# Kernel optimization log

Hardware: AMD Instinct MI355X
Metric: run time of the kernel (lower is better)

Reference implementation:

```python
import jax, jax.numpy as jnp
import numpy as np

DIM = 2048
HID = 1024
E = 16
TOP_K = 2
S_SHARED = 2


def setup_inputs() -> dict:
    key = jax.random.key(0)
    ks = jax.random.split(key, 6)
    scale = 0.02
    x = jax.random.normal(ks[0], (2, 2048, DIM), dtype=jnp.float32)
    gate_w = jax.random.normal(ks[1], (DIM, E), dtype=jnp.float32) * scale
    shared_w1 = jax.random.normal(ks[2], (S_SHARED, DIM, HID), dtype=jnp.float32) * scale
    shared_w2 = jax.random.normal(ks[3], (S_SHARED, HID, DIM), dtype=jnp.float32) * scale
    w1 = jax.random.normal(ks[4], (E, DIM, HID), dtype=jnp.float32) * scale
    w2 = jax.random.normal(ks[5], (E, HID, DIM), dtype=jnp.float32) * scale
    return {"x": x, "gate_w": gate_w, "shared_w1": shared_w1,
            "shared_w2": shared_w2, "w1": w1, "w2": w2}


def reference(x, gate_w, shared_w1, shared_w2, w1, w2):
    orig_shape = x.shape
    xf = x.reshape(-1, orig_shape[-1])  # [T, D]

    # Shared experts: sum of SiLU MLPs
    hs = jax.nn.silu(jnp.einsum('td,sdh->sth', xf, shared_w1))
    shared_out = jnp.einsum('sth,shd->td', hs, shared_w2)

    # Gating
    probs = jax.nn.softmax(xf @ gate_w, axis=-1)              # [T, E]
    weights, indices = jax.lax.top_k(probs, TOP_K)            # [T, K]
    weights = weights / weights.sum(axis=-1, keepdims=True)
    aux_loss = (probs.mean(axis=0) ** 2).sum() * E

    # Combine weights per (token, expert): top_k indices are distinct
    combine = (jax.nn.one_hot(indices, E, dtype=xf.dtype) *
               weights[..., None]).sum(axis=1)                # [T, E]

    # Dense all-expert compute (reference form of gather-GEMM-scatter)
    h = jax.nn.silu(jnp.einsum('td,edh->eth', xf, w1))        # [E, T, H]
    y = jnp.einsum('eth,ehd->etd', h, w2)                     # [E, T, D]
    routed_out = jnp.einsum('te,etd->td', combine, y)         # [T, D]

    out = (shared_out + routed_out).reshape(orig_shape)
    return out, aux_loss
```

## Files before the change

### kernel.cpp

```cpp
#include <hip/hip_runtime.h>
#include <math.h>

typedef unsigned short u16;
typedef __bf16 bf16x8 __attribute__((ext_vector_type(8)));
typedef float f32x4 __attribute__((ext_vector_type(4)));

#define T_TOK 4096
#define DIMD 2048
#define HIDD 1024
#define NEXP 16
#define RMAX 10240
#define MAXBLK 96
#define BM 128
#define BN 128
#define BK 32

__device__ __forceinline__ u16 f2b(float f) {
  unsigned u = __builtin_bit_cast(unsigned, f);
  unsigned r = (u + 0x7FFFu + ((u >> 16) & 1u)) >> 16;
  return (u16)r;
}

__device__ __forceinline__ void gld16(const void* g, void* l) {
  __builtin_amdgcn_global_load_lds(
      (const __attribute__((address_space(1))) void*)g,
      (__attribute__((address_space(3))) void*)l, 16, 0, 0);
}


__global__ void k_init(int* perm, int* cnt, int* fill) {
  int i = blockIdx.x * blockDim.x + threadIdx.x;
  if (i < RMAX) perm[i] = -1;
  if (i < NEXP) { cnt[i] = 0; fill[i] = 0; }
}

__global__ void k_cvt(const float* __restrict__ x, u16* __restrict__ xb) {
  const int i = blockIdx.x * blockDim.x + threadIdx.x;
  const float4 v = ((const float4*)x)[i];
  union { u16 u[4]; unsigned long long q; } t;
  t.u[0] = f2b(v.x); t.u[1] = f2b(v.y); t.u[2] = f2b(v.z); t.u[3] = f2b(v.w);
  ((unsigned long long*)xb)[i] = t.q;
}

__global__ __launch_bounds__(256)
void k_tr(const float* __restrict__ W, u16* __restrict__ Wt,
          int K, int N, long estride, int ld_out) {
  __shared__ float t[64][65];
  const int e = blockIdx.z;
  const float* Win = W + (size_t)e * (size_t)K * (size_t)N;
  u16* Wo = Wt + (size_t)e * (size_t)estride;
  const int n0 = blockIdx.x * 64, k0 = blockIdx.y * 64;
  const int r = threadIdx.x >> 4;
  const int c = (threadIdx.x & 15) * 4;
#pragma unroll
  for (int p = 0; p < 4; ++p) {
    const int kk = p * 16 + r;
    const float4 v = *(const float4*)&Win[(size_t)(k0 + kk) * N + n0 + c];
    t[kk][c] = v.x; t[kk][c + 1] = v.y; t[kk][c + 2] = v.z; t[kk][c + 3] = v.w;
  }
  __syncthreads();
#pragma unroll
  for (int p = 0; p < 4; ++p) {
    const int nn = p * 16 + r;
    ushort4 o;
    o.x = f2b(t[c + 0][nn]); o.y = f2b(t[c + 1][nn]);
    o.z = f2b(t[c + 2][nn]); o.w = f2b(t[c + 3][nn]);
    *(ushort4*)&Wo[(size_t)(n0 + nn) * ld_out + k0 + c] = o;
  }
}

__global__ __launch_bounds__(256)
void k_gate(const float* __restrict__ x, const float* __restrict__ gw,
            int* __restrict__ top2i, float* __restrict__ top2w,
            int* __restrict__ cnt, float* __restrict__ partial) {
  const int e = threadIdx.x & 15;
  const int tt = threadIdx.x >> 4;
  const int t = blockIdx.x * 16 + tt;
  const float* xp = x + (size_t)t * DIMD;
  float acc = 0.f;
#pragma unroll 8
  for (int k = 0; k < DIMD; ++k) acc = fmaf(xp[k], gw[k * NEXP + e], acc);
  __shared__ float lg[16][17];
  __shared__ float pr[16][17];
  lg[tt][e] = acc;
  __syncthreads();
  if (e == 0) {
    float l[16];
    float mx = -1e30f;
    for (int j = 0; j < 16; ++j) { l[j] = lg[tt][j]; mx = fmaxf(mx, l[j]); }
    float s = 0.f;
    for (int j = 0; j < 16; ++j) { l[j] = expf(l[j] - mx); s += l[j]; }
    const float inv = 1.f / s;
    float p1 = -1.f, p2 = -1.f; int i1 = 0, i2 = 0;
    for (int j = 0; j < 16; ++j) {
      const float p = l[j] * inv;
      pr[tt][j] = p;
      if (p > p1) { p2 = p1; i2 = i1; p1 = p; i1 = j; }
      else if (p > p2) { p2 = p; i2 = j; }
    }
    const float wsum = p1 + p2;
    top2i[t * 2 + 0] = i1;
    top2i[t * 2 + 1] = i2;
    top2w[t * 2 + 0] = p1 / wsum;
    top2w[t * 2 + 1] = p2 / wsum;
    atomicAdd(&cnt[i1], 1);
    atomicAdd(&cnt[i2], 1);
  }
  __syncthreads();
  if (tt == 0) {
    float s = 0.f;
    for (int j = 0; j < 16; ++j) s += pr[j][e];
    partial[blockIdx.x * 16 + e] = s;
  }
}

__global__ __launch_bounds__(256)
void k_aux(const float* __restrict__ partial, float* __restrict__ auxOut) {
  __shared__ float s[16][17];
  const int e = threadIdx.x & 15, c = threadIdx.x >> 4;
  float a = 0.f;
  for (int b = c; b < 256; b += 16) a += partial[b * 16 + e];
  s[c][e] = a;
  __syncthreads();
  if (threadIdx.x == 0) {
    float aux = 0.f;
    for (int j = 0; j < 16; ++j) {
      float tot = 0.f;
      for (int cc = 0; cc < 16; ++cc) tot += s[cc][j];
      const float m = tot / (float)T_TOK;
      aux += m * m;
    }
    auxOut[0] = aux * (float)NEXP;
  }
}

__global__ void k_off(const int* __restrict__ cnt, int* __restrict__ offs,
                      int* __restrict__ tbl_e, int* __restrict__ tbl_r0,
                      int* __restrict__ nblk) {
  if (threadIdx.x != 0 || blockIdx.x != 0) return;
  int o = 0, nb = 0;
  for (int e = 0; e < NEXP; ++e) {
    offs[e] = o;
    const int b = (cnt[e] + BM - 1) / BM;
    for (int i = 0; i < b; ++i) { tbl_e[nb] = e; tbl_r0[nb] = o + i * BM; ++nb; }
    o += b * BM;
  }
  offs[NEXP] = o;
  nblk[0] = nb;
}

__global__ void k_fill(const int* __restrict__ top2i, const float* __restrict__ top2w,
                       const int* __restrict__ offs, int* __restrict__ fill,
                       int* __restrict__ perm, float* __restrict__ wrow) {
  const int id = blockIdx.x * blockDim.x + threadIdx.x;
  if (id >= T_TOK * 2) return;
  const int e = top2i[id];
  const int pos = atomicAdd(&fill[e], 1);
  const int r = offs[e] + pos;
  perm[r] = id >> 1;
  wrow[r] = top2w[id];
}

template<int MODE>
__global__ __launch_bounds__(256)
void k_gemm(const u16* __restrict__ A, const u16* __restrict__ Bt,
            void* __restrict__ Outp,
            const int* __restrict__ perm, const float* __restrict__ wrow,
            const int* __restrict__ tbl_e, const int* __restrict__ tbl_r0,
            const int* __restrict__ nblk,
            int K, int lda, int ldb, size_t bstride) {
  __shared__ u16 As[BM * BK];
  __shared__ u16 Bs[BN * BK];

  const int bx = blockIdx.x, by = blockIdx.y;
  int expert = 0, r0;
  if (MODE == 2 || MODE == 3) {
    if (bx >= *nblk) return;
    expert = tbl_e[bx];
    r0 = tbl_r0[bx];
  } else {
    r0 = bx * BM;
    if (MODE == 0) expert = blockIdx.z;
  }
  const u16* B = Bt + (size_t)expert * bstride;

  const int tid = threadIdx.x;
  const int w = tid >> 6, lane = tid & 63;
  const int lr = lane >> 2;
  const int lk = (lane & 3) * 8;

  int ra0 = r0 + w * 32 + lr, ra1 = ra0 + 16;
  if (MODE == 2) {
    const int p0 = perm[ra0]; ra0 = (p0 < 0) ? 0 : p0;
    const int p1 = perm[ra1]; ra1 = (p1 < 0) ? 0 : p1;
  }
  const int n0 = by * BN;
  const u16* ap0 = A + (size_t)ra0 * lda + lk;
  const u16* ap1 = A + (size_t)ra1 * lda + lk;
  const u16* bp0 = B + (size_t)(n0 + w * 32 + lr) * ldb + lk;
  const u16* bp1 = bp0 + (size_t)16 * ldb;
  u16* lA0 = &As[w * 1024];
  u16* lA1 = &As[w * 1024 + 512];
  u16* lB0 = &Bs[w * 1024];
  u16* lB1 = &Bs[w * 1024 + 512];

  f32x4 acc[4][4];
#pragma unroll
  for (int i = 0; i < 4; ++i)
#pragma unroll
    for (int j = 0; j < 4; ++j) {
      acc[i][j][0] = 0.f; acc[i][j][1] = 0.f; acc[i][j][2] = 0.f; acc[i][j][3] = 0.f;
    }

  const int wr = (w >> 1) * 64, wc = (w & 1) * 64;
  const int lm = lane & 15, lq = lane >> 4;
  const u16* aRd = &As[(wr + lm) * BK + lq * 8];
  const u16* bRd = &Bs[(wc + lm) * BK + lq * 8];

  for (int k0 = 0; k0 < K; k0 += BK) {
    gld16(ap0 + k0, lA0);
    gld16(ap1 + k0, lA1);
    gld16(bp0 + k0, lB0);
    gld16(bp1 + k0, lB1);
    __syncthreads();
    bf16x8 af[4], bq[4];
#pragma unroll
    for (int i = 0; i < 4; ++i) af[i] = *(const bf16x8*)(aRd + i * 16 * BK);
#pragma unroll
    for (int j = 0; j < 4; ++j) bq[j] = *(const bf16x8*)(bRd + j * 16 * BK);
#pragma unroll
    for (int i = 0; i < 4; ++i)
#pragma unroll
      for (int j = 0; j < 4; ++j)
        acc[i][j] = __builtin_amdgcn_mfma_f32_16x16x32_bf16(af[i], bq[j], acc[i][j], 0, 0, 0);
    __syncthreads();
  }

  u16* outB16 = (u16*)Outp;
  float* outF = (float*)Outp;
#pragma unroll
  for (int i = 0; i < 4; ++i) {
    const int lr0 = wr + i * 16 + lq * 4;
#pragma unroll
    for (int j = 0; j < 4; ++j) {
      const int gc = n0 + wc + j * 16 + lm;
#pragma unroll
      for (int r = 0; r < 4; ++r) {
        const float v = acc[i][j][r];
        const int lrow = lr0 + r;
        if (MODE == 0) {
          const float s = v / (1.f + expf(-v));
          outB16[(size_t)(r0 + lrow) * DIMD + expert * HIDD + gc] = f2b(s);
        } else if (MODE == 2) {
          const float s = v / (1.f + expf(-v));
          outB16[(size_t)(r0 + lrow) * HIDD + gc] = f2b(s);
        } else if (MODE == 1) {
          outF[(size_t)(r0 + lrow) * DIMD + gc] = v;
        } else {
          const int rr = r0 + lrow;
          const int t = perm[rr];
          if (t >= 0) atomicAdd(&outF[(size_t)t * DIMD + gc], wrow[rr] * v);
        }
      }
    }
  }
}


extern "C" void kernel_launch(void* const* d_in, const int* in_sizes, int n_in,
                              void* d_out, int out_size, void* d_ws, size_t ws_size,
                              hipStream_t stream) {
  const float* x   = (const float*)d_in[0];
  const float* gw  = (const float*)d_in[1];
  const float* sw1 = (const float*)d_in[2];
  const float* sw2 = (const float*)d_in[3];
  const float* w1  = (const float*)d_in[4];
  const float* w2  = (const float*)d_in[5];
  float* out = (float*)d_out;

  char* ws = (char*)d_ws;
  u16* xb    = (u16*)(ws);
  u16* hbS   = (u16*)(ws + (size_t)( 16 << 20));
  u16* hbR   = (u16*)(ws + (size_t)( 32 << 20));
  u16* sw1t  = (u16*)(ws + (size_t)( 52 << 20));
  u16* sw2ct = (u16*)(ws + (size_t)( 60 << 20));
  u16* w1t   = (u16*)(ws + (size_t)( 68 << 20));
  u16* w2t   = (u16*)(ws + (size_t)(132 << 20));
  char* p = ws + (size_t)(196 << 20);
  int*   top2i   = (int*)p;    p += T_TOK * 2 * 4;
  float* top2w   = (float*)p;  p += T_TOK * 2 * 4;
  int*   perm    = (int*)p;    p += RMAX * 4;
  float* wrow    = (float*)p;  p += RMAX * 4;
  int*   cnt     = (int*)p;    p += 16 * 4;
  int*   fill    = (int*)p;    p += 16 * 4;
  int*   offs    = (int*)p;    p += 32 * 4;
  int*   tbl_e   = (int*)p;    p += MAXBLK * 4;
  int*   tbl_r0  = (int*)p;    p += MAXBLK * 4;
  int*   nblk    = (int*)p;    p += 16 * 4;
  float* partial = (float*)p;  p += 256 * 16 * 4;

  k_init<<<(RMAX + 255) / 256, 256, 0, stream>>>(perm, cnt, fill);
  k_cvt<<<(T_TOK * DIMD / 4) / 256, 256, 0, stream>>>(x, xb);
  k_gate<<<T_TOK / 16, 256, 0, stream>>>(x, gw, top2i, top2w, cnt, partial);
  k_off<<<1, 64, 0, stream>>>(cnt, offs, tbl_e, tbl_r0, nblk);
  k_fill<<<(T_TOK * 2 + 255) / 256, 256, 0, stream>>>(top2i, top2w, offs, fill, perm, wrow);
  k_aux<<<1, 256, 0, stream>>>(partial, out + (size_t)T_TOK * DIMD);

  k_tr<<<dim3(1024 / 64, 2048 / 64,  2), 256, 0, stream>>>(sw1, sw1t, 2048, 1024, 1024l * 2048, 2048);
  k_tr<<<dim3(2048 / 64, 1024 / 64,  2), 256, 0, stream>>>(sw2, sw2ct, 1024, 2048, 1024, 2048);
  k_tr<<<dim3(1024 / 64, 2048 / 64, 16), 256, 0, stream>>>(w1, w1t, 2048, 1024, 1024l * 2048, 2048);
  k_tr<<<dim3(2048 / 64, 1024 / 64, 16), 256, 0, stream>>>(w2, w2t, 1024, 2048, 2048l * 1024, 1024);

  k_gemm<0><<<dim3(32, 8, 2), 256, 0, stream>>>(xb, sw1t, hbS,
      nullptr, nullptr, nullptr, nullptr, nullptr, 2048, 2048, 2048, (size_t)1024 * 2048);
  k_gemm<1><<<dim3(32, 16, 1), 256, 0, stream>>>(hbS, sw2ct, out,
      nullptr, nullptr, nullptr, nullptr, nullptr, 2048, 2048, 2048, 0);
  k_gemm<2><<<dim3(80, 8, 1), 256, 0, stream>>>(xb, w1t, hbR,
      perm, nullptr, tbl_e, tbl_r0, nblk, 2048, 2048, 2048, (size_t)1024 * 2048);
  k_gemm<3><<<dim3(80, 16, 1), 256, 0, stream>>>(hbR, w2t, out,
      perm, wrow, tbl_e, tbl_r0, nblk, 1024, 1024, 1024, (size_t)2048 * 1024);
}
```

Baseline: 861.4 us.

## Merge shared and routed expert GEMMs into combined up and down launches

Replaces four separate GEMM launches with two kernels: one computes both shared and routed up-projections in a single grid, and one computes both down-projections, writing everything via atomicAdd into an output that is zeroed up front. The aim is to fill the GPU better by running the shared and routed work concurrently and to cut launch count and tail effects. The cost is an extra zeroing pass over the output and atomic adds for the shared-expert results, which were previously plain stores. Blocks with different K lengths in the down kernel may also cause load imbalance.

```diff
diff --git a/kernel.cpp b/kernel.cpp
--- a/kernel.cpp
+++ b/kernel.cpp
@@ -27,6 +27,12 @@
       (__attribute__((address_space(3))) void*)l, 16, 0, 0);
 }
 
+
+__global__ void k_zero(float* __restrict__ o) {
+  const int i = blockIdx.x * blockDim.x + threadIdx.x;
+  float4 z = {0.f, 0.f, 0.f, 0.f};
+  ((float4*)o)[i] = z;
+}
 
 __global__ void k_init(int* perm, int* cnt, int* fill) {
   int i = blockIdx.x * blockDim.x + threadIdx.x;
@@ -161,62 +167,11 @@
   wrow[r] = top2w[id];
 }
 
-template<int MODE>
-__global__ __launch_bounds__(256)
-void k_gemm(const u16* __restrict__ A, const u16* __restrict__ Bt,
-            void* __restrict__ Outp,
-            const int* __restrict__ perm, const float* __restrict__ wrow,
-            const int* __restrict__ tbl_e, const int* __restrict__ tbl_r0,
-            const int* __restrict__ nblk,
-            int K, int lda, int ldb, size_t bstride) {
-  __shared__ u16 As[BM * BK];
-  __shared__ u16 Bs[BN * BK];
-
-  const int bx = blockIdx.x, by = blockIdx.y;
-  int expert = 0, r0;
-  if (MODE == 2 || MODE == 3) {
-    if (bx >= *nblk) return;
-    expert = tbl_e[bx];
-    r0 = tbl_r0[bx];
-  } else {
-    r0 = bx * BM;
-    if (MODE == 0) expert = blockIdx.z;
-  }
-  const u16* B = Bt + (size_t)expert * bstride;
-
-  const int tid = threadIdx.x;
-  const int w = tid >> 6, lane = tid & 63;
-  const int lr = lane >> 2;
-  const int lk = (lane & 3) * 8;
-
-  int ra0 = r0 + w * 32 + lr, ra1 = ra0 + 16;
-  if (MODE == 2) {
-    const int p0 = perm[ra0]; ra0 = (p0 < 0) ? 0 : p0;
-    const int p1 = perm[ra1]; ra1 = (p1 < 0) ? 0 : p1;
-  }
-  const int n0 = by * BN;
-  const u16* ap0 = A + (size_t)ra0 * lda + lk;
-  const u16* ap1 = A + (size_t)ra1 * lda + lk;
-  const u16* bp0 = B + (size_t)(n0 + w * 32 + lr) * ldb + lk;
-  const u16* bp1 = bp0 + (size_t)16 * ldb;
-  u16* lA0 = &As[w * 1024];
-  u16* lA1 = &As[w * 1024 + 512];
-  u16* lB0 = &Bs[w * 1024];
-  u16* lB1 = &Bs[w * 1024 + 512];
-
-  f32x4 acc[4][4];
-#pragma unroll
-  for (int i = 0; i < 4; ++i)
-#pragma unroll
-    for (int j = 0; j < 4; ++j) {
-      acc[i][j][0] = 0.f; acc[i][j][1] = 0.f; acc[i][j][2] = 0.f; acc[i][j][3] = 0.f;
-    }
-
-  const int wr = (w >> 1) * 64, wc = (w & 1) * 64;
-  const int lm = lane & 15, lq = lane >> 4;
-  const u16* aRd = &As[(wr + lm) * BK + lq * 8];
-  const u16* bRd = &Bs[(wc + lm) * BK + lq * 8];
-
+__device__ __forceinline__ void gemm_core(
+    const u16* __restrict__ ap0, const u16* __restrict__ ap1,
+    const u16* __restrict__ bp0, const u16* __restrict__ bp1, int K,
+    u16* lA0, u16* lA1, u16* lB0, u16* lB1,
+    const u16* aRd, const u16* bRd, f32x4 (&acc)[4][4]) {
   for (int k0 = 0; k0 < K; k0 += BK) {
     gld16(ap0 + k0, lA0);
     gld16(ap1 + k0, lA1);
@@ -235,31 +190,156 @@
         acc[i][j] = __builtin_amdgcn_mfma_f32_16x16x32_bf16(af[i], bq[j], acc[i][j], 0, 0, 0);
     __syncthreads();
   }
-
-  u16* outB16 = (u16*)Outp;
-  float* outF = (float*)Outp;
+}
+
+__global__ __launch_bounds__(256)
+void k_up(const u16* __restrict__ xb, const u16* __restrict__ sw1t,
+          const u16* __restrict__ w1t, u16* __restrict__ hbS,
+          u16* __restrict__ hbR, const int* __restrict__ perm,
+          const int* __restrict__ tbl_e, const int* __restrict__ tbl_r0,
+          const int* __restrict__ nblk) {
+  __shared__ u16 As[BM * BK];
+  __shared__ u16 Bs[BN * BK];
+
+  const int bx = blockIdx.x, by = blockIdx.y;
+  const int tid = threadIdx.x;
+  const int w = tid >> 6, lane = tid & 63;
+  const int lr = lane >> 2;
+  const int lk = (lane & 3) * 8;
+
+  const bool routed = bx >= 64;
+  int expert, r0, ra0, ra1;
+  const u16* B;
+  if (!routed) {
+    expert = bx >> 5;
+    r0 = (bx & 31) * BM;
+    B = sw1t + (size_t)expert * (size_t)HIDD * DIMD;
+    ra0 = r0 + w * 32 + lr; ra1 = ra0 + 16;
+  } else {
+    const int rbx = bx - 64;
+    if (rbx >= *nblk) return;
+    expert = tbl_e[rbx];
+    r0 = tbl_r0[rbx];
+    B = w1t + (size_t)expert * (size_t)HIDD * DIMD;
+    const int rr0 = r0 + w * 32 + lr, rr1 = rr0 + 16;
+    const int p0 = perm[rr0]; ra0 = (p0 < 0) ? 0 : p0;
+    const int p1 = perm[rr1]; ra1 = (p1 < 0) ? 0 : p1;
+  }
+
+  const int n0 = by * BN;
+  const u16* ap0 = xb + (size_t)ra0 * DIMD + lk;
+  const u16* ap1 = xb + (size_t)ra1 * DIMD + lk;
+  const u16* bp0 = B + (size_t)(n0 + w * 32 + lr) * DIMD + lk;
+  const u16* bp1 = bp0 + (size_t)16 * DIMD;
+  u16* lA0 = &As[w * 1024];
+  u16* lA1 = &As[w * 1024 + 512];
+  u16* lB0 = &Bs[w * 1024];
+  u16* lB1 = &Bs[w * 1024 + 512];
+
+  f32x4 acc[4][4];
+#pragma unroll
+  for (int i = 0; i < 4; ++i)
+#pragma unroll
+    for (int j = 0; j < 4; ++j) {
+      acc[i][j][0] = 0.f; acc[i][j][1] = 0.f; acc[i][j][2] = 0.f; acc[i][j][3] = 0.f;
+    }
+
+  const int wr = (w >> 1) * 64, wc = (w & 1) * 64;
+  const int lm = lane & 15, lq = lane >> 4;
+  const u16* aRd = &As[(wr + lm) * BK + lq * 8];
+  const u16* bRd = &Bs[(wc + lm) * BK + lq * 8];
+
+  gemm_core(ap0, ap1, bp0, bp1, DIMD, lA0, lA1, lB0, lB1, aRd, bRd, acc);
+
 #pragma unroll
   for (int i = 0; i < 4; ++i) {
-    const int lr0 = wr + i * 16 + lq * 4;
+#pragma unroll
+    for (int r = 0; r < 4; ++r) {
+      const int row = r0 + wr + i * 16 + lq * 4 + r;
+      u16* dst = routed ? &hbR[(size_t)row * HIDD]
+                        : &hbS[(size_t)row * DIMD + expert * HIDD];
+#pragma unroll
+      for (int j = 0; j < 4; ++j) {
+        const int gc = n0 + wc + j * 16 + lm;
+        const float v = acc[i][j][r];
+        const float s = v / (1.f + expf(-v));
+        dst[gc] = f2b(s);
+      }
+    }
+  }
+}
+
+__global__ __launch_bounds__(256)
+void k_down(const u16* __restrict__ hbS, const u16* __restrict__ hbR,
+            const u16* __restrict__ sw2ct, const u16* __restrict__ w2t,
+            float* __restrict__ out, const int* __restrict__ perm,
+            const float* __restrict__ wrow,
+            const int* __restrict__ tbl_e, const int* __restrict__ tbl_r0,
+            const int* __restrict__ nblk) {
+  __shared__ u16 As[BM * BK];
+  __shared__ u16 Bs[BN * BK];
+
+  const int bx = blockIdx.x, by = blockIdx.y;
+  const int tid = threadIdx.x;
+  const int w = tid >> 6, lane = tid & 63;
+  const int lr = lane >> 2;
+  const int lk = (lane & 3) * 8;
+
+  const bool routed = bx >= 32;
+  int r0, K, ld;
+  const u16 *Amat, *B;
+  if (!routed) {
+    r0 = bx * BM;
+    Amat = hbS; K = DIMD; ld = DIMD;
+    B = sw2ct;
+  } else {
+    const int rbx = bx - 32;
+    if (rbx >= *nblk) return;
+    const int expert = tbl_e[rbx];
+    r0 = tbl_r0[rbx];
+    Amat = hbR; K = HIDD; ld = HIDD;
+    B = w2t + (size_t)expert * (size_t)DIMD * HIDD;
+  }
+
+  const int n0 = by * BN;
+  const u16* ap0 = Amat + (size_t)(r0 + w * 32 + lr) * ld + lk;
+  const u16* ap1 = ap0 + (size_t)16 * ld;
+  const u16* bp0 = B + (size_t)(n0 + w * 32 + lr) * ld + lk;
+  const u16* bp1 = bp0 + (size_t)16 * ld;
+  u16* lA0 = &As[w * 1024];
+  u16* lA1 = &As[w * 1024 + 512];
+  u16* lB0 = &Bs[w * 1024];
+  u16* lB1 = &Bs[w * 1024 + 512];
+
+  f32x4 acc[4][4];
+#pragma unroll
+  for (int i = 0; i < 4; ++i)
 #pragma unroll
     for (int j = 0; j < 4; ++j) {
-      const int gc = n0 + wc + j * 16 + lm;
-#pragma unroll
-      for (int r = 0; r < 4; ++r) {
-        const float v = acc[i][j][r];
-        const int lrow = lr0 + r;
-        if (MODE == 0) {
-          const float s = v / (1.f + expf(-v));
-          outB16[(size_t)(r0 + lrow) * DIMD + expert * HIDD + gc] = f2b(s);
-        } else if (MODE == 2) {
-          const float s = v / (1.f + expf(-v));
-          outB16[(size_t)(r0 + lrow) * HIDD + gc] = f2b(s);
-        } else if (MODE == 1) {
-          outF[(size_t)(r0 + lrow) * DIMD + gc] = v;
-        } else {
-          const int rr = r0 + lrow;
-          const int t = perm[rr];
-          if (t >= 0) atomicAdd(&outF[(size_t)t * DIMD + gc], wrow[rr] * v);
+      acc[i][j][0] = 0.f; acc[i][j][1] = 0.f; acc[i][j][2] = 0.f; acc[i][j][3] = 0.f;
+    }
+
+  const int wr = (w >> 1) * 64, wc = (w & 1) * 64;
+  const int lm = lane & 15, lq = lane >> 4;
+  const u16* aRd = &As[(wr + lm) * BK + lq * 8];
+  const u16* bRd = &Bs[(wc + lm) * BK + lq * 8];
+
+  gemm_core(ap0, ap1, bp0, bp1, K, lA0, lA1, lB0, lB1, aRd, bRd, acc);
+
+#pragma unroll
+  for (int i = 0; i < 4; ++i) {
+#pragma unroll
+    for (int r = 0; r < 4; ++r) {
+      const int rr = r0 + wr + i * 16 + lq * 4 + r;
+      int t; float wt;
+      if (!routed) { t = rr; wt = 1.f; }
+      else { t = perm[rr]; wt = (t >= 0) ? wrow[rr] : 0.f; }
+      if (t >= 0) {
+        float* dst = &out[(size_t)t * DIMD];
+#pragma unroll
+        for (int j = 0; j < 4; ++j) {
+          const int gc = n0 + wc + j * 16 + lm;
+          atomicAdd(&dst[gc], wt * acc[i][j][r]);
         }
       }
     }
@@ -299,6 +379,7 @@
   int*   nblk    = (int*)p;    p += 16 * 4;
   float* partial = (float*)p;  p += 256 * 16 * 4;
 
+  k_zero<<<(T_TOK * DIMD / 4) / 256, 256, 0, stream>>>(out);
   k_init<<<(RMAX + 255) / 256, 256, 0, stream>>>(perm, cnt, fill);
   k_cvt<<<(T_TOK * DIMD / 4) / 256, 256, 0, stream>>>(x, xb);
   k_gate<<<T_TOK / 16, 256, 0, stream>>>(x, gw, top2i, top2w, cnt, partial);
@@ -311,12 +392,8 @@
   k_tr<<<dim3(1024 / 64, 2048 / 64, 16), 256, 0, stream>>>(w1, w1t, 2048, 1024, 1024l * 2048, 2048);
   k_tr<<<dim3(2048 / 64, 1024 / 64, 16), 256, 0, stream>>>(w2, w2t, 1024, 2048, 2048l * 1024, 1024);
 
-  k_gemm<0><<<dim3(32, 8, 2), 256, 0, stream>>>(xb, sw1t, hbS,
-      nullptr, nullptr, nullptr, nullptr, nullptr, 2048, 2048, 2048, (size_t)1024 * 2048);
-  k_gemm<1><<<dim3(32, 16, 1), 256, 0, stream>>>(hbS, sw2ct, out,
-      nullptr, nullptr, nullptr, nullptr, nullptr, 2048, 2048, 2048, 0);
-  k_gemm<2><<<dim3(80, 8, 1), 256, 0, stream>>>(xb, w1t, hbR,
-      perm, nullptr, tbl_e, tbl_r0, nblk, 2048, 2048, 2048, (size_t)1024 * 2048);
-  k_gemm<3><<<dim3(80, 16, 1), 256, 0, stream>>>(hbR, w2t, out,
-      perm, wrow, tbl_e, tbl_r0, nblk, 1024, 1024, 1024, (size_t)2048 * 1024);
-}
+  k_up<<<dim3(64 + 80, 8), 256, 0, stream>>>(xb, sw1t, w1t, hbS, hbR,
+                                             perm, tbl_e, tbl_r0, nblk);
+  k_down<<<dim3(32 + 80, 16), 256, 0, stream>>>(hbS, hbR, sw2ct, w2t, out,
+                                                perm, wrow, tbl_e, tbl_r0, nblk);
+}
```

Result: faster. 826.0 us (-4.1%).
